# Kernel tuning notes

Hardware: AMD Instinct MI355X
Metric: run time of the kernel (lower is better)

## Reference

```python
import jax, jax.numpy as jnp
import numpy as np

EPS = 1e-08
C_CHANNELS = 4  # fixed number of mask labels (mask.max()+1 in the torch code)


def _sample_nearest(vol, g):
    """torch.grid_sample(mode='nearest', padding_mode='zeros', align_corners=True).
    vol: (X,Y,Z); g: (...,3) normalized coords in [-1,1], grid order (x,y,z)
    maps to volume axes (X,Y,Z) (the torch code permutes the volume to (Z,Y,X)
    so that grid x->X, y->Y, z->Z)."""
    X, Y, Z = vol.shape
    sizes = jnp.array([X, Y, Z], dtype=g.dtype)
    idx = jnp.round((g + 1.0) * 0.5 * (sizes - 1.0))   # align_corners=True unnormalize
    valid = jnp.all((idx >= 0) & (idx <= sizes - 1.0), axis=-1)
    ii = jnp.clip(idx, 0, sizes - 1.0).astype(jnp.int32)
    vals = vol[ii[..., 0], ii[..., 1], ii[..., 2]]
    return jnp.where(valid, vals, jnp.zeros((), vals.dtype))


def _forward(volume, source, target, mask):
    X, Y, Z = volume.shape
    dims = jnp.array([X, Y, Z], dtype=volume.dtype)
    sd = target - source + EPS                                   # (B,D,3)

    def plane_alphas(n, axis):
        planes = jnp.arange(n + 1, dtype=volume.dtype) - 0.5     # plane coords
        return (planes[None, None, :] - source[..., axis:axis + 1]) / sd[..., axis:axis + 1]

    alphas = jnp.concatenate(
        [plane_alphas(X, 0), plane_alphas(Y, 1), plane_alphas(Z, 2)], axis=-1)
    alphas = jnp.sort(alphas, axis=-1)                           # (B,D,S)
    alphamid = 0.5 * (alphas[..., :-1] + alphas[..., 1:])        # (B,D,S-1)

    # XYZ midpoints, normalized to [-1,1] grid coords
    xyz = source[:, :, None, :] + alphamid[..., None] * sd[:, :, None, :]
    g = 2.0 * xyz / dims - 1.0                                   # (B,D,S-1,3)

    img = _sample_nearest(volume, g) * jnp.diff(alphas, axis=-1)  # (B,D,S-1)

    # per-segment channel labels, scatter-add into C channels
    ch = _sample_nearest(mask, g).astype(jnp.int32)              # (B,D,S-1)
    B, D, _ = img.shape
    bb = jnp.arange(B)[:, None, None]
    dd = jnp.arange(D)[None, :, None]
    out = jnp.zeros((B, D, C_CHANNELS), img.dtype).at[bb, dd, ch].add(img)
    out = jnp.transpose(out, (0, 2, 1))                          # (B,C,D)

    raylength = jnp.linalg.norm(sd, axis=-1)                     # (B,D)
    return out * raylength[:, None, :]


def setup_inputs() -> dict:
    key = jax.random.key(0)
    k1, k2, k3, k4 = jax.random.split(key, 4)
    B, D = 2, 16384
    XYZ = (256, 256, 256)
    volume = jax.random.uniform(k1, XYZ, dtype=jnp.float32)
    # mask labels in [0, C) stored as float, as in the torch module
    mask = jax.random.randint(k2, XYZ, 0, C_CHANNELS).astype(jnp.float32)
    # sources in front of the volume, targets behind it -> rays traverse volume
    source = jax.random.uniform(k3, (B, D, 3), dtype=jnp.float32) * 20.0 - 120.0
    target = jax.random.uniform(k4, (B, D, 3), dtype=jnp.float32) * 20.0 + 360.0
    return {"volume": volume, "source": source, "target": target, "mask": mask}


def reference(volume, source, target, mask):
    return _forward(volume, source, target, mask)
```

## Files before the change

### kernel.cpp

```cpp
#include <hip/hip_runtime.h>
#include <math.h>

#define NRAYS 32768
#define D_DIM 16384
#define NVOX 256
#define NCH 4
#define CHUNKS 16
#define RAYS_PER_BLOCK 15

#define SLAB_HALF 64
#define SLAB_W 128
#define SLAB_CELLS (256 * SLAB_W * SLAB_W)

#define GROUPS 32
#define GROUP_RAYS 1024

#define SLAB_BYTES ((size_t)SLAB_CELLS * 4)
#define OFF_SIDX   (SLAB_BYTES)
#define SIDX_BYTES ((size_t)CHUNKS * NRAYS * 4)
#define OFF_PART   (OFF_SIDX + SIDX_BYTES)
#define PART_BYTES ((size_t)CHUNKS * NRAYS * 16)
#define WS_NEED    (OFF_PART + PART_BYTES)

__device__ __forceinline__ float alpha_of(int i, float s, float sd) {
    float p = __fsub_rn((float)i, 0.5f);
    return __fdiv_rn(__fsub_rn(p, s), sd);
}
__device__ __forceinline__ float alpha_of_f(float fi, float s, float sd) {
    float p = __fsub_rn(fi, 0.5f);
    return __fdiv_rn(__fsub_rn(p, s), sd);
}
__device__ __forceinline__ int cnt_less(float t, float s, float sd) {
    float est = __fadd_rn(__fadd_rn(__fmul_rn(t, sd), s), 0.5f);
    int i = (int)floorf(est) - 2;
    if (i < 0) i = 0;
    if (i > 257) i = 257;
    while (i <= 256 && alpha_of(i, s, sd) < t) ++i;
    return i;
}

__device__ __forceinline__ float rcp_refine(float sd) {
    float rc = __builtin_amdgcn_rcpf(sd);
    float e0 = __fmaf_rn(-sd, rc, 1.0f);
    return __fmaf_rn(e0, rc, rc);
}
__device__ __forceinline__ float div_m(float num, float sd, float r0) {
    float q0 = __fmul_rn(num, r0);
    float e1 = __fmaf_rn(-sd, q0, num);
    float q1 = __fmaf_rn(e1, r0, q0);
    float e2 = __fmaf_rn(-sd, q1, num);
    return __fmaf_rn(e2, r0, q1);
}

__global__ __launch_bounds__(256) void pack_kernel(
    const float* __restrict__ vol, const float* __restrict__ msk,
    unsigned int* __restrict__ packed)
{
    const int idx = blockIdx.x * 256 + threadIdx.x;
    const int lz = idx & (SLAB_W - 1);
    const int ly = (idx >> 7) & (SLAB_W - 1);
    const int x  = idx >> 14;
    const int y = x + ly - SLAB_HALF;
    const int z = x + lz - SLAB_HALF;
    unsigned int v = 0u;
    if ((unsigned)y < 256u && (unsigned)z < 256u) {
        const int o = (x << 16) | (y << 8) | z;
        const unsigned int u = __float_as_uint(vol[o]) & ~3u;
        v = u | ((unsigned int)msk[o] & 3u);
    }
    packed[idx] = v;
}

__global__ __launch_bounds__(256) void sort_kernel(
    const float* __restrict__ src, const float* __restrict__ tgt,
    int* __restrict__ sidx)
{
    __shared__ unsigned int bins[4096];
    __shared__ unsigned int psum[256];
    const int t = threadIdx.x;
    const int c = blockIdx.x >> 5;
    const int g = blockIdx.x & (GROUPS - 1);
    const int base = g * GROUP_RAYS;

    for (int j = t; j < 4096; j += 256) bins[j] = 0u;
    __syncthreads();

    int key[4];
    const float xc = (float)(16 * c) + 7.5f;
    for (int j = 0; j < 4; ++j) {
        const int r = base + j * 256 + t;
        const float sx = src[r*3+0], sy = src[r*3+1], sz = src[r*3+2];
        const float sdx = tgt[r*3+0] - sx + 1e-8f;
        const float sdy = tgt[r*3+1] - sy + 1e-8f;
        const float sdz = tgt[r*3+2] - sz + 1e-8f;
        const float a = (xc - sx) / sdx;
        const float y = sy + a * sdy;
        const float z = sz + a * sdz;
        int ky = (int)((y - xc + 64.0f) * 0.5f); ky = min(max(ky, 0), 63);
        int kz = (int)((z - xc + 64.0f) * 0.5f); kz = min(max(kz, 0), 63);
        key[j] = (ky << 6) | kz;
        atomicAdd(&bins[key[j]], 1u);
    }
    __syncthreads();

    unsigned int run = 0;
    for (int j = 0; j < 16; ++j) run += bins[t * 16 + j];
    psum[t] = run;
    __syncthreads();
    for (int off = 1; off < 256; off <<= 1) {
        unsigned int v = (t >= off) ? psum[t - off] : 0u;
        __syncthreads();
        psum[t] += v;
        __syncthreads();
    }
    unsigned int acc = psum[t] - run;
    for (int j = 0; j < 16; ++j) {
        unsigned int v = bins[t * 16 + j];
        bins[t * 16 + j] = acc;
        acc += v;
    }
    __syncthreads();

    for (int j = 0; j < 4; ++j) {
        const int r = base + j * 256 + t;
        const unsigned int pos = atomicAdd(&bins[key[j]], 1u);
        sidx[(size_t)c * NRAYS + base + pos] = r;
    }
}

__global__ __launch_bounds__(256) void trace_kernel(
    const float* __restrict__ src, const float* __restrict__ tgt,
    const unsigned int* __restrict__ packed,
    const int* __restrict__ sidx,
    float* __restrict__ partials)
{
    const int c   = blockIdx.x >> 7;
    const int sub = blockIdx.x & 127;

    const int r = sidx[(size_t)c * NRAYS + sub * 256 + threadIdx.x];

    const float sx = src[r*3+0], sy = src[r*3+1], sz = src[r*3+2];
    const float sdx = __fadd_rn(__fsub_rn(tgt[r*3+0], sx), 1e-8f);
    const float sdy = __fadd_rn(__fsub_rn(tgt[r*3+1], sy), 1e-8f);
    const float sdz = __fadd_rn(__fsub_rn(tgt[r*3+2], sz), 1e-8f);

    const float INF = __int_as_float(0x7f800000);

    const float fi_start = (c == 0) ? -1.0f : (float)(16 * c);
    const float stopf    = (c == 15) ? 1.0e9f : (float)(16 * (c + 1));

    float fxi = fi_start;
    float ax = alpha_of_f(fxi, sx, sdx);
    const int iy0 = cnt_less(ax, sy, sdy);
    const int iz0 = cnt_less(ax, sz, sdz);
    float fyi = (float)iy0, fzi = (float)iz0;
    float ay = (iy0 <= NVOX) ? alpha_of_f(fyi, sy, sdy) : INF;
    float az = (iz0 <= NVOX) ? alpha_of_f(fzi, sz, sdz) : INF;

    const float rcx = rcp_refine(sdx);
    const float rcy = rcp_refine(sdy);
    const float rcz = rcp_refine(sdz);

    const float sx7 = __fmul_rn(sx, 0.0078125f);
    const float sy7 = __fmul_rn(sy, 0.0078125f);
    const float sz7 = __fmul_rn(sz, 0.0078125f);
    const float sdx7 = __fmul_rn(sdx, 0.0078125f);
    const float sdy7 = __fmul_rn(sdy, 0.0078125f);
    const float sdz7 = __fmul_rn(sdz, 0.0078125f);

    float acc0 = 0.f, acc1 = 0.f, acc2 = 0.f, acc3 = 0.f;

    float a_prev = ax;
    {
        fxi = __fadd_rn(fxi, 1.0f);
        const float num = __fsub_rn(__fsub_rn(fxi, 0.5f), sx);
        ax = div_m(num, sdx, rcx);
    }

    for (int it = 0; it < 840; ++it) {
        const float t = fminf(fminf(ax, ay), az);
        if (t == INF) break;

        const bool ex = (t == ax);
        const bool ey = !ex && (t == ay);
        const bool ez = !ex && !ey;

        const float fi_old = ex ? fxi : (ey ? fyi : fzi);
        const bool stop = ex && (fi_old == stopf);

        const float fi_n = __fadd_rn(fi_old, 1.0f);
        const float s_s  = ex ? sx  : (ey ? sy  : sz);
        const float sd_s = ex ? sdx : (ey ? sdy : sdz);
        const float r_s  = ex ? rcx : (ey ? rcy : rcz);
        const float num  = __fsub_rn(__fsub_rn(fi_n, 0.5f), s_s);
        float a_n = div_m(num, sd_s, r_s);
        a_n = (fi_n <= 256.0f) ? a_n : INF;

        fxi = ex ? fi_n : fxi;  ax = ex ? a_n : ax;
        fyi = ey ? fi_n : fyi;  ay = ey ? a_n : ay;
        fzi = ez ? fi_n : fzi;  az = ez ? a_n : az;

        const float diff = __fsub_rn(t, a_prev);
        const float mid  = __fmul_rn(0.5f, __fadd_rn(a_prev, t));
        const float px7 = __fadd_rn(sx7, __fmul_rn(mid, sdx7));
        const float py7 = __fadd_rn(sy7, __fmul_rn(mid, sdy7));
        const float pz7 = __fadd_rn(sz7, __fmul_rn(mid, sdz7));
        const float hx = __fadd_rn(__fsub_rn(px7, 1.0f), 1.0f);
        const float hy = __fadd_rn(__fsub_rn(py7, 1.0f), 1.0f);
        const float hz = __fadd_rn(__fsub_rn(pz7, 1.0f), 1.0f);
        const float fxr = rintf(__fmul_rn(hx, 127.5f));
        const float fyr = rintf(__fmul_rn(hy, 127.5f));
        const float fzr = rintf(__fmul_rn(hz, 127.5f));
        const int vx = (int)fxr, vy = (int)fyr, vz = (int)fzr;

        if ((unsigned)vx < 256u) {
            const int ry = vy - vx + SLAB_HALF;
            const int rz = vz - vx + SLAB_HALF;
            const unsigned int bits = packed[(vx << 14) | (ry << 7) | rz];
            const float val = __uint_as_float(bits & ~3u);
            const int ch = (int)(bits & 3u);
            const float img = __fmul_rn(val, diff);
            acc0 += (ch == 0) ? img : 0.f;
            acc1 += (ch == 1) ? img : 0.f;
            acc2 += (ch == 2) ? img : 0.f;
            acc3 += (ch == 3) ? img : 0.f;
        }

        if (stop) break;
        a_prev = t;
    }

    float4* p4 = (float4*)(partials + ((size_t)c * NRAYS + r) * 4);
    *p4 = make_float4(acc0, acc1, acc2, acc3);
}

__global__ __launch_bounds__(256) void reduce_kernel(
    const float* __restrict__ src, const float* __restrict__ tgt,
    const float* __restrict__ partials, float* __restrict__ out)
{
    const int id = blockIdx.x * 256 + threadIdx.x;
    if (id >= NRAYS * NCH) return;
    const int r  = id >> 2;
    const int ch = id & 3;
    float s = 0.f;
    for (int c = 0; c < CHUNKS; ++c)
        s = __fadd_rn(s, partials[((size_t)c * NRAYS + r) * 4 + ch]);
    const float sx = src[r*3+0], sy = src[r*3+1], sz = src[r*3+2];
    const float sdx = __fadd_rn(__fsub_rn(tgt[r*3+0], sx), 1e-8f);
    const float sdy = __fadd_rn(__fsub_rn(tgt[r*3+1], sy), 1e-8f);
    const float sdz = __fadd_rn(__fsub_rn(tgt[r*3+2], sz), 1e-8f);
    const float rlen = sqrtf(__fadd_rn(__fadd_rn(
        __fmul_rn(sdx, sdx), __fmul_rn(sdy, sdy)), __fmul_rn(sdz, sdz)));
    const int b = r >> 14;
    const int d = r & (D_DIM - 1);
    out[((size_t)b * NCH + ch) * D_DIM + d] = __fmul_rn(s, rlen);
}

template<int USE_PACKED>
__global__ __launch_bounds__(256) void siddon_kernel(
    const float* __restrict__ volume, const float* __restrict__ src,
    const float* __restrict__ tgt, const float* __restrict__ maskv,
    const unsigned int* __restrict__ packed, float* __restrict__ out)
{
    __shared__ float partials[RAYS_PER_BLOCK * 17][NCH + 1];
    const int tid = threadIdx.x;
    const int rl = tid / 17;
    const int ck = tid - rl * 17;
    const long ray = (long)blockIdx.x * RAYS_PER_BLOCK + rl;
    float acc0 = 0.f, acc1 = 0.f, acc2 = 0.f, acc3 = 0.f;

    if (tid < RAYS_PER_BLOCK * 17 && ray < NRAYS) {
        const float sx = src[ray*3+0], sy = src[ray*3+1], sz = src[ray*3+2];
        const float sdx = __fadd_rn(__fsub_rn(tgt[ray*3+0], sx), 1e-8f);
        const float sdy = __fadd_rn(__fsub_rn(tgt[ray*3+1], sy), 1e-8f);
        const float sdz = __fadd_rn(__fsub_rn(tgt[ray*3+2], sz), 1e-8f);
        int ix, iy, iz, stopx;
        if (ck == 0) { ix = 0; iy = 0; iz = 0; stopx = 0; }
        else {
            const int cc = ck - 1;
            ix = 16 * cc;
            const float t0 = alpha_of(ix, sx, sdx);
            iy = cnt_less(t0, sy, sdy);
            iz = cnt_less(t0, sz, sdz);
            stopx = (cc == 15) ? 1000 : 16 * (cc + 1);
        }
        const float INF = __int_as_float(0x7f800000);
        const float INV256 = 0.00390625f;
        float fx_i = (float)ix, fy_i = (float)iy, fz_i = (float)iz;
        float ax = (ix <= NVOX) ? alpha_of_f(fx_i, sx, sdx) : INF;
        float ay = (iy <= NVOX) ? alpha_of_f(fy_i, sy, sdy) : INF;
        float az = (iz <= NVOX) ? alpha_of_f(fz_i, sz, sdz) : INF;
        float a_prev = 0.f; bool first = true;
        for (int it = 0; it < 840; ++it) {
            int m; float t;
            if (ax <= ay && ax <= az) { m = 0; t = ax; }
            else if (ay <= az)        { m = 1; t = ay; }
            else                      { m = 2; t = az; }
            if (t == INF) break;
            const bool stop = (m == 0 && ix == stopx);
            if (m == 0) { ++ix; fx_i = __fadd_rn(fx_i, 1.0f);
                ax = (ix <= NVOX) ? alpha_of_f(fx_i, sx, sdx) : INF; }
            else if (m == 1) { ++iy; fy_i = __fadd_rn(fy_i, 1.0f);
                ay = (iy <= NVOX) ? alpha_of_f(fy_i, sy, sdy) : INF; }
            else { ++iz; fz_i = __fadd_rn(fz_i, 1.0f);
                az = (iz <= NVOX) ? alpha_of_f(fz_i, sz, sdz) : INF; }
            if (!first) {
                const float diff = __fsub_rn(t, a_prev);
                const float mid  = __fmul_rn(0.5f, __fadd_rn(a_prev, t));
                const float px = __fadd_rn(sx, __fmul_rn(mid, sdx));
                const float py = __fadd_rn(sy, __fmul_rn(mid, sdy));
                const float pz = __fadd_rn(sz, __fmul_rn(mid, sdz));
                const float gx = __fsub_rn(__fmul_rn(__fmul_rn(2.0f, px), INV256), 1.0f);
                const float gy = __fsub_rn(__fmul_rn(__fmul_rn(2.0f, py), INV256), 1.0f);
                const float gz = __fsub_rn(__fmul_rn(__fmul_rn(2.0f, pz), INV256), 1.0f);
                const float fx = rintf(__fmul_rn(__fmul_rn(__fadd_rn(gx, 1.0f), 0.5f), 255.0f));
                const float fy = rintf(__fmul_rn(__fmul_rn(__fadd_rn(gy, 1.0f), 0.5f), 255.0f));
                const float fz = rintf(__fmul_rn(__fmul_rn(__fadd_rn(gz, 1.0f), 0.5f), 255.0f));
                if (fx >= 0.f && fx <= 255.f && fy >= 0.f && fy <= 255.f &&
                    fz >= 0.f && fz <= 255.f) {
                    const int vx = (int)fx, vy = (int)fy, vz = (int)fz;
                    float val; int ch;
                    if (USE_PACKED) {
                        const int ry = vy - vx + SLAB_HALF;
                        const int rz = vz - vx + SLAB_HALF;
                        if ((unsigned)ry < (unsigned)SLAB_W && (unsigned)rz < (unsigned)SLAB_W) {
                            const unsigned int bits = packed[(vx << 14) | (ry << 7) | rz];
                            val = __uint_as_float(bits & ~3u);
                            ch = (int)(bits & 3u);
                        } else {
                            const int off = (vx << 16) | (vy << 8) | vz;
                            val = volume[off]; ch = (int)maskv[off];
                        }
                    } else {
                        const int off = (vx << 16) | (vy << 8) | vz;
                        val = volume[off]; ch = (int)maskv[off];
                    }
                    const float img = __fmul_rn(val, diff);
                    acc0 += (ch == 0) ? img : 0.f;
                    acc1 += (ch == 1) ? img : 0.f;
                    acc2 += (ch == 2) ? img : 0.f;
                    acc3 += (ch == 3) ? img : 0.f;
                }
            }
            if (stop) break;
            a_prev = t; first = false;
        }
    }
    if (tid < RAYS_PER_BLOCK * 17) {
        partials[tid][0] = acc0; partials[tid][1] = acc1;
        partials[tid][2] = acc2; partials[tid][3] = acc3;
    }
    __syncthreads();
    if (tid < RAYS_PER_BLOCK * NCH) {
        const int rl2 = tid >> 2;
        const int ch  = tid & 3;
        const long ray2 = (long)blockIdx.x * RAYS_PER_BLOCK + rl2;
        if (ray2 < NRAYS) {
            float s = 0.f;
            for (int k = 0; k < 17; ++k)
                s = __fadd_rn(s, partials[rl2 * 17 + k][ch]);
            const float sx = src[ray2*3+0], sy = src[ray2*3+1], sz = src[ray2*3+2];
            const float sdx = __fadd_rn(__fsub_rn(tgt[ray2*3+0], sx), 1e-8f);
            const float sdy = __fadd_rn(__fsub_rn(tgt[ray2*3+1], sy), 1e-8f);
            const float sdz = __fadd_rn(__fsub_rn(tgt[ray2*3+2], sz), 1e-8f);
            const float rlen = sqrtf(__fadd_rn(__fadd_rn(
                __fmul_rn(sdx, sdx), __fmul_rn(sdy, sdy)), __fmul_rn(sdz, sdz)));
            const int b = (int)(ray2 >> 14);
            const int d = (int)(ray2 & (D_DIM - 1));
            out[((long)b * NCH + ch) * D_DIM + d] = __fmul_rn(s, rlen);
        }
    }
}

extern "C" void kernel_launch(void* const* d_in, const int* in_sizes, int n_in,
                              void* d_out, int out_size, void* d_ws, size_t ws_size,
                              hipStream_t stream) {
    const float* volume = (const float*)d_in[0];
    const float* src    = (const float*)d_in[1];
    const float* tgt    = (const float*)d_in[2];
    const float* maskv  = (const float*)d_in[3];
    float* out = (float*)d_out;
    char* ws = (char*)d_ws;

    unsigned int* packed = (unsigned int*)(ws);

    if (ws_size >= WS_NEED) {
        int*   sidx = (int*)(ws + OFF_SIDX);
        float* part = (float*)(ws + OFF_PART);

        pack_kernel<<<SLAB_CELLS / 256, 256, 0, stream>>>(volume, maskv, packed);
        sort_kernel<<<CHUNKS * GROUPS, 256, 0, stream>>>(src, tgt, sidx);
        trace_kernel<<<CHUNKS * 128, 256, 0, stream>>>(src, tgt, packed, sidx, part);
        reduce_kernel<<<(NRAYS * NCH) / 256, 256, 0, stream>>>(src, tgt, part, out);
    } else if (ws_size >= SLAB_BYTES) {
        const int nblocks = (NRAYS + RAYS_PER_BLOCK - 1) / RAYS_PER_BLOCK;
        pack_kernel<<<SLAB_CELLS / 256, 256, 0, stream>>>(volume, maskv, packed);
        siddon_kernel<1><<<nblocks, 256, 0, stream>>>(volume, src, tgt, maskv, packed, out);
    } else {
        const int nblocks = (NRAYS + RAYS_PER_BLOCK - 1) / RAYS_PER_BLOCK;
        siddon_kernel<0><<<nblocks, 256, 0, stream>>>(volume, src, tgt, maskv, packed, out);
    }
}
```

Before: 83.29 us.

## Split ray traversal into 17 chunks, use LDS accumulators, precompute plane offsets

Raises the chunk count from 16 to 17 so the last x-plane range gets its own chunk, and guards the first next-alpha with the 256-plane bound. Replaces the four per-channel register accumulators with per-thread shared-memory slots updated by atomicAdd, and folds the -0.5-s subtraction into a precomputed per-axis constant. This aims to cut VALU selects and register pressure in the inner loop. The cost is an LDS atomic on every segment, and the 17th chunk needs the host launch config and workspace sizing to match.

```diff
diff --git a/kernel.cpp b/kernel.cpp
--- a/kernel.cpp
+++ b/kernel.cpp
@@ -5,7 +5,7 @@
 #define D_DIM 16384
 #define NVOX 256
 #define NCH 4
-#define CHUNKS 16
+#define CHUNKS 17
 #define RAYS_PER_BLOCK 15
 
 #define SLAB_HALF 64
@@ -134,10 +134,16 @@
     const int* __restrict__ sidx,
     float* __restrict__ partials)
 {
+    __shared__ float sacc[256 * 5];
+    const int tid = threadIdx.x;
+    const int sbase = tid * 5;
+    sacc[sbase + 0] = 0.f; sacc[sbase + 1] = 0.f;
+    sacc[sbase + 2] = 0.f; sacc[sbase + 3] = 0.f;
+
     const int c   = blockIdx.x >> 7;
     const int sub = blockIdx.x & 127;
 
-    const int r = sidx[(size_t)c * NRAYS + sub * 256 + threadIdx.x];
+    const int r = sidx[(size_t)c * NRAYS + sub * 256 + tid];
 
     const float sx = src[r*3+0], sy = src[r*3+1], sz = src[r*3+2];
     const float sdx = __fadd_rn(__fsub_rn(tgt[r*3+0], sx), 1e-8f);
@@ -147,7 +153,7 @@
     const float INF = __int_as_float(0x7f800000);
 
     const float fi_start = (c == 0) ? -1.0f : (float)(16 * c);
-    const float stopf    = (c == 15) ? 1.0e9f : (float)(16 * (c + 1));
+    const float stopf    = (c >= 16) ? 1.0e9f : (float)(16 * (c + 1));
 
     float fxi = fi_start;
     float ax = alpha_of_f(fxi, sx, sdx);
@@ -160,6 +166,9 @@
     const float rcx = rcp_refine(sdx);
     const float rcy = rcp_refine(sdy);
     const float rcz = rcp_refine(sdz);
+    const float Bx = __fsub_rn(-0.5f, sx);
+    const float By = __fsub_rn(-0.5f, sy);
+    const float Bz = __fsub_rn(-0.5f, sz);
 
     const float sx7 = __fmul_rn(sx, 0.0078125f);
     const float sy7 = __fmul_rn(sy, 0.0078125f);
@@ -168,13 +177,12 @@
     const float sdy7 = __fmul_rn(sdy, 0.0078125f);
     const float sdz7 = __fmul_rn(sdz, 0.0078125f);
 
-    float acc0 = 0.f, acc1 = 0.f, acc2 = 0.f, acc3 = 0.f;
-
     float a_prev = ax;
     {
         fxi = __fadd_rn(fxi, 1.0f);
-        const float num = __fsub_rn(__fsub_rn(fxi, 0.5f), sx);
-        ax = div_m(num, sdx, rcx);
+        const float num = __fadd_rn(fxi, Bx);
+        const float axn = div_m(num, sdx, rcx);
+        ax = (fxi <= 256.0f) ? axn : INF;
     }
 
     for (int it = 0; it < 840; ++it) {
@@ -189,10 +197,10 @@
         const bool stop = ex && (fi_old == stopf);
 
         const float fi_n = __fadd_rn(fi_old, 1.0f);
-        const float s_s  = ex ? sx  : (ey ? sy  : sz);
+        const float B_s  = ex ? Bx  : (ey ? By  : Bz);
         const float sd_s = ex ? sdx : (ey ? sdy : sdz);
         const float r_s  = ex ? rcx : (ey ? rcy : rcz);
-        const float num  = __fsub_rn(__fsub_rn(fi_n, 0.5f), s_s);
+        const float num  = __fadd_rn(fi_n, B_s);
         float a_n = div_m(num, sd_s, r_s);
         a_n = (fi_n <= 256.0f) ? a_n : INF;
 
@@ -220,10 +228,7 @@
             const float val = __uint_as_float(bits & ~3u);
             const int ch = (int)(bits & 3u);
             const float img = __fmul_rn(val, diff);
-            acc0 += (ch == 0) ? img : 0.f;
-            acc1 += (ch == 1) ? img : 0.f;
-            acc2 += (ch == 2) ? img : 0.f;
-            acc3 += (ch == 3) ? img : 0.f;
+            atomicAdd(&sacc[sbase + ch], img);
         }
 
         if (stop) break;
@@ -231,7 +236,8 @@
     }
 
     float4* p4 = (float4*)(partials + ((size_t)c * NRAYS + r) * 4);
-    *p4 = make_float4(acc0, acc1, acc2, acc3);
+    *p4 = make_float4(sacc[sbase + 0], sacc[sbase + 1],
+                      sacc[sbase + 2], sacc[sbase + 3]);
 }
 
 __global__ __launch_bounds__(256) void reduce_kernel(
```

Measured after the change: 155.0 us. 86.1% more time.

## Trace two interleaved rays per thread and add a seventeenth chunk

Applied to the files above, without the earlier changes.

Each thread now steps two independent rays in the same loop, so two memory gathers can be in flight per iteration and load latency is hidden better. The block count is halved to match. The chunk count goes from 16 to 17, and the last chunk's stop condition changes to c >= 16, presumably to split the tail of each ray further. The plane-alpha numerator is precomputed as (-0.5 - s) per axis, which saves one subtraction per step. The risks are higher register pressure with lower occupancy, divergence when the paired rays finish at different times, and a larger scratch buffer and more partial sums to reduce.

```diff
diff --git a/kernel.cpp b/kernel.cpp
--- a/kernel.cpp
+++ b/kernel.cpp
@@ -5,7 +5,7 @@
 #define D_DIM 16384
 #define NVOX 256
 #define NCH 4
-#define CHUNKS 16
+#define CHUNKS 17
 #define RAYS_PER_BLOCK 15
 
 #define SLAB_HALF 64
@@ -128,110 +128,139 @@
     }
 }
 
+struct RayState {
+    float sx, sy, sz, sdx, sdy, sdz;
+    float rcx, rcy, rcz, Bx, By, Bz;
+    float sx7, sy7, sz7, sdx7, sdy7, sdz7;
+    float fxi, fyi, fzi, ax, ay, az;
+    float a_prev, stopf;
+    float acc0, acc1, acc2, acc3;
+    int r;
+};
+
+__device__ __forceinline__ void ray_init(RayState& S,
+    const float* __restrict__ src, const float* __restrict__ tgt, int r, int c)
+{
+    S.r = r;
+    const float INF = __int_as_float(0x7f800000);
+    S.sx = src[r*3+0]; S.sy = src[r*3+1]; S.sz = src[r*3+2];
+    S.sdx = __fadd_rn(__fsub_rn(tgt[r*3+0], S.sx), 1e-8f);
+    S.sdy = __fadd_rn(__fsub_rn(tgt[r*3+1], S.sy), 1e-8f);
+    S.sdz = __fadd_rn(__fsub_rn(tgt[r*3+2], S.sz), 1e-8f);
+
+    const float fi_start = (c == 0) ? -1.0f : (float)(16 * c);
+    S.stopf = (c >= 16) ? 1.0e9f : (float)(16 * (c + 1));
+
+    S.fxi = fi_start;
+    S.ax = alpha_of_f(S.fxi, S.sx, S.sdx);
+    const int iy0 = cnt_less(S.ax, S.sy, S.sdy);
+    const int iz0 = cnt_less(S.ax, S.sz, S.sdz);
+    S.fyi = (float)iy0; S.fzi = (float)iz0;
+    S.ay = (iy0 <= NVOX) ? alpha_of_f(S.fyi, S.sy, S.sdy) : INF;
+    S.az = (iz0 <= NVOX) ? alpha_of_f(S.fzi, S.sz, S.sdz) : INF;
+
+    S.rcx = rcp_refine(S.sdx); S.rcy = rcp_refine(S.sdy); S.rcz = rcp_refine(S.sdz);
+    S.Bx = __fsub_rn(-0.5f, S.sx);
+    S.By = __fsub_rn(-0.5f, S.sy);
+    S.Bz = __fsub_rn(-0.5f, S.sz);
+    S.sx7 = __fmul_rn(S.sx, 0.0078125f);
+    S.sy7 = __fmul_rn(S.sy, 0.0078125f);
+    S.sz7 = __fmul_rn(S.sz, 0.0078125f);
+    S.sdx7 = __fmul_rn(S.sdx, 0.0078125f);
+    S.sdy7 = __fmul_rn(S.sdy, 0.0078125f);
+    S.sdz7 = __fmul_rn(S.sdz, 0.0078125f);
+    S.acc0 = 0.f; S.acc1 = 0.f; S.acc2 = 0.f; S.acc3 = 0.f;
+
+    S.a_prev = S.ax;
+    S.fxi = __fadd_rn(S.fxi, 1.0f);
+    const float num = __fadd_rn(S.fxi, S.Bx);
+    const float axn = div_m(num, S.sdx, S.rcx);
+    S.ax = (S.fxi <= 256.0f) ? axn : INF;
+}
+
+__device__ __forceinline__ bool ray_step(RayState& S,
+    const unsigned int* __restrict__ packed)
+{
+    const float INF = __int_as_float(0x7f800000);
+    const float t = fminf(fminf(S.ax, S.ay), S.az);
+    if (t == INF) return true;
+
+    const bool ex = (t == S.ax);
+    const bool ey = !ex && (t == S.ay);
+    const bool ez = !ex && !ey;
+
+    const float fi_old = ex ? S.fxi : (ey ? S.fyi : S.fzi);
+    const bool stop = ex && (fi_old == S.stopf);
+
+    const float fi_n = __fadd_rn(fi_old, 1.0f);
+    const float B_s  = ex ? S.Bx  : (ey ? S.By  : S.Bz);
+    const float sd_s = ex ? S.sdx : (ey ? S.sdy : S.sdz);
+    const float r_s  = ex ? S.rcx : (ey ? S.rcy : S.rcz);
+    const float num  = __fadd_rn(fi_n, B_s);
+    float a_n = div_m(num, sd_s, r_s);
+    a_n = (fi_n <= 256.0f) ? a_n : INF;
+
+    S.fxi = ex ? fi_n : S.fxi;  S.ax = ex ? a_n : S.ax;
+    S.fyi = ey ? fi_n : S.fyi;  S.ay = ey ? a_n : S.ay;
+    S.fzi = ez ? fi_n : S.fzi;  S.az = ez ? a_n : S.az;
+
+    const float diff = __fsub_rn(t, S.a_prev);
+    const float mid  = __fmul_rn(0.5f, __fadd_rn(S.a_prev, t));
+    const float px7 = __fadd_rn(S.sx7, __fmul_rn(mid, S.sdx7));
+    const float py7 = __fadd_rn(S.sy7, __fmul_rn(mid, S.sdy7));
+    const float pz7 = __fadd_rn(S.sz7, __fmul_rn(mid, S.sdz7));
+    const float hx = __fadd_rn(__fsub_rn(px7, 1.0f), 1.0f);
+    const float hy = __fadd_rn(__fsub_rn(py7, 1.0f), 1.0f);
+    const float hz = __fadd_rn(__fsub_rn(pz7, 1.0f), 1.0f);
+    const float fxr = rintf(__fmul_rn(hx, 127.5f));
+    const float fyr = rintf(__fmul_rn(hy, 127.5f));
+    const float fzr = rintf(__fmul_rn(hz, 127.5f));
+    const int vx = (int)fxr, vy = (int)fyr, vz = (int)fzr;
+
+    if ((unsigned)vx < 256u) {
+        const int ry = vy - vx + SLAB_HALF;
+        const int rz = vz - vx + SLAB_HALF;
+        const unsigned int bits = packed[(vx << 14) | (ry << 7) | rz];
+        const float val = __uint_as_float(bits & ~3u);
+        const int ch = (int)(bits & 3u);
+        const float img = __fmul_rn(val, diff);
+        S.acc0 += (ch == 0) ? img : 0.f;
+        S.acc1 += (ch == 1) ? img : 0.f;
+        S.acc2 += (ch == 2) ? img : 0.f;
+        S.acc3 += (ch == 3) ? img : 0.f;
+    }
+
+    if (stop) return true;
+    S.a_prev = t;
+    return false;
+}
+
 __global__ __launch_bounds__(256) void trace_kernel(
     const float* __restrict__ src, const float* __restrict__ tgt,
     const unsigned int* __restrict__ packed,
     const int* __restrict__ sidx,
     float* __restrict__ partials)
 {
-    const int c   = blockIdx.x >> 7;
-    const int sub = blockIdx.x & 127;
-
-    const int r = sidx[(size_t)c * NRAYS + sub * 256 + threadIdx.x];
-
-    const float sx = src[r*3+0], sy = src[r*3+1], sz = src[r*3+2];
-    const float sdx = __fadd_rn(__fsub_rn(tgt[r*3+0], sx), 1e-8f);
-    const float sdy = __fadd_rn(__fsub_rn(tgt[r*3+1], sy), 1e-8f);
-    const float sdz = __fadd_rn(__fsub_rn(tgt[r*3+2], sz), 1e-8f);
-
-    const float INF = __int_as_float(0x7f800000);
-
-    const float fi_start = (c == 0) ? -1.0f : (float)(16 * c);
-    const float stopf    = (c == 15) ? 1.0e9f : (float)(16 * (c + 1));
-
-    float fxi = fi_start;
-    float ax = alpha_of_f(fxi, sx, sdx);
-    const int iy0 = cnt_less(ax, sy, sdy);
-    const int iz0 = cnt_less(ax, sz, sdz);
-    float fyi = (float)iy0, fzi = (float)iz0;
-    float ay = (iy0 <= NVOX) ? alpha_of_f(fyi, sy, sdy) : INF;
-    float az = (iz0 <= NVOX) ? alpha_of_f(fzi, sz, sdz) : INF;
-
-    const float rcx = rcp_refine(sdx);
-    const float rcy = rcp_refine(sdy);
-    const float rcz = rcp_refine(sdz);
-
-    const float sx7 = __fmul_rn(sx, 0.0078125f);
-    const float sy7 = __fmul_rn(sy, 0.0078125f);
-    const float sz7 = __fmul_rn(sz, 0.0078125f);
-    const float sdx7 = __fmul_rn(sdx, 0.0078125f);
-    const float sdy7 = __fmul_rn(sdy, 0.0078125f);
-    const float sdz7 = __fmul_rn(sdz, 0.0078125f);
-
-    float acc0 = 0.f, acc1 = 0.f, acc2 = 0.f, acc3 = 0.f;
-
-    float a_prev = ax;
-    {
-        fxi = __fadd_rn(fxi, 1.0f);
-        const float num = __fsub_rn(__fsub_rn(fxi, 0.5f), sx);
-        ax = div_m(num, sdx, rcx);
-    }
-
-    for (int it = 0; it < 840; ++it) {
-        const float t = fminf(fminf(ax, ay), az);
-        if (t == INF) break;
-
-        const bool ex = (t == ax);
-        const bool ey = !ex && (t == ay);
-        const bool ez = !ex && !ey;
-
-        const float fi_old = ex ? fxi : (ey ? fyi : fzi);
-        const bool stop = ex && (fi_old == stopf);
-
-        const float fi_n = __fadd_rn(fi_old, 1.0f);
-        const float s_s  = ex ? sx  : (ey ? sy  : sz);
-        const float sd_s = ex ? sdx : (ey ? sdy : sdz);
-        const float r_s  = ex ? rcx : (ey ? rcy : rcz);
-        const float num  = __fsub_rn(__fsub_rn(fi_n, 0.5f), s_s);
-        float a_n = div_m(num, sd_s, r_s);
-        a_n = (fi_n <= 256.0f) ? a_n : INF;
-
-        fxi = ex ? fi_n : fxi;  ax = ex ? a_n : ax;
-        fyi = ey ? fi_n : fyi;  ay = ey ? a_n : ay;
-        fzi = ez ? fi_n : fzi;  az = ez ? a_n : az;
-
-        const float diff = __fsub_rn(t, a_prev);
-        const float mid  = __fmul_rn(0.5f, __fadd_rn(a_prev, t));
-        const float px7 = __fadd_rn(sx7, __fmul_rn(mid, sdx7));
-        const float py7 = __fadd_rn(sy7, __fmul_rn(mid, sdy7));
-        const float pz7 = __fadd_rn(sz7, __fmul_rn(mid, sdz7));
-        const float hx = __fadd_rn(__fsub_rn(px7, 1.0f), 1.0f);
-        const float hy = __fadd_rn(__fsub_rn(py7, 1.0f), 1.0f);
-        const float hz = __fadd_rn(__fsub_rn(pz7, 1.0f), 1.0f);
-        const float fxr = rintf(__fmul_rn(hx, 127.5f));
-        const float fyr = rintf(__fmul_rn(hy, 127.5f));
-        const float fzr = rintf(__fmul_rn(hz, 127.5f));
-        const int vx = (int)fxr, vy = (int)fyr, vz = (int)fzr;
-
-        if ((unsigned)vx < 256u) {
-            const int ry = vy - vx + SLAB_HALF;
-            const int rz = vz - vx + SLAB_HALF;
-            const unsigned int bits = packed[(vx << 14) | (ry << 7) | rz];
-            const float val = __uint_as_float(bits & ~3u);
-            const int ch = (int)(bits & 3u);
-            const float img = __fmul_rn(val, diff);
-            acc0 += (ch == 0) ? img : 0.f;
-            acc1 += (ch == 1) ? img : 0.f;
-            acc2 += (ch == 2) ? img : 0.f;
-            acc3 += (ch == 3) ? img : 0.f;
-        }
-
-        if (stop) break;
-        a_prev = t;
-    }
-
-    float4* p4 = (float4*)(partials + ((size_t)c * NRAYS + r) * 4);
-    *p4 = make_float4(acc0, acc1, acc2, acc3);
+    const int c   = blockIdx.x >> 6;
+    const int sub = blockIdx.x & 63;
+
+    const int rA = sidx[(size_t)c * NRAYS + sub * 512 + threadIdx.x];
+    const int rB = sidx[(size_t)c * NRAYS + sub * 512 + 256 + threadIdx.x];
+
+    RayState A, B;
+    ray_init(A, src, tgt, rA, c);
+    ray_init(B, src, tgt, rB, c);
+
+    bool dA = false, dB = false;
+    for (int it = 0; it < 840 && !(dA && dB); ++it) {
+        if (!dA) dA = ray_step(A, packed);
+        if (!dB) dB = ray_step(B, packed);
+    }
+
+    float4* pA = (float4*)(partials + ((size_t)c * NRAYS + A.r) * 4);
+    *pA = make_float4(A.acc0, A.acc1, A.acc2, A.acc3);
+    float4* pB = (float4*)(partials + ((size_t)c * NRAYS + B.r) * 4);
+    *pB = make_float4(B.acc0, B.acc1, B.acc2, B.acc3);
 }
 
 __global__ __launch_bounds__(256) void reduce_kernel(
@@ -390,7 +419,7 @@
 
         pack_kernel<<<SLAB_CELLS / 256, 256, 0, stream>>>(volume, maskv, packed);
         sort_kernel<<<CHUNKS * GROUPS, 256, 0, stream>>>(src, tgt, sidx);
-        trace_kernel<<<CHUNKS * 128, 256, 0, stream>>>(src, tgt, packed, sidx, part);
+        trace_kernel<<<CHUNKS * 64, 256, 0, stream>>>(src, tgt, packed, sidx, part);
         reduce_kernel<<<(NRAYS * NCH) / 256, 256, 0, stream>>>(src, tgt, part, out);
     } else if (ws_size >= SLAB_BYTES) {
         const int nblocks = (NRAYS + RAYS_PER_BLOCK - 1) / RAYS_PER_BLOCK;
```

Measured after the change: 151.4 us. 81.7% more time.
